# Kernel tuning notes

Measured on AMD Instinct MI355X. Metric: run time of the kernel, lower is better.

The kernel has to match this reference:

```python
import jax, jax.numpy as jnp
import numpy as np

NH = 8
QCH = 256
KCH = 256
VCH = 256


def setup_inputs() -> dict:
    key = jax.random.key(0)
    ks = jax.random.split(key, 6)
    B, C, H, W = 8, 512, 28, 28
    return {
        "inputs": jax.random.normal(ks[0], (B, C, H, W), jnp.float32),
        "inputs_st": jax.random.normal(ks[1], (B, C, H, W), jnp.float32),
        "Wq": jax.random.normal(ks[2], (QCH, C), jnp.float32) * 0.02,
        "bq": jnp.zeros((QCH,), jnp.float32),
        "Wkv": jax.random.normal(ks[3], (KCH + VCH, C), jnp.float32) * 0.02,
        "bkv": jnp.zeros((KCH + VCH,), jnp.float32),
        "Wo": jax.random.normal(ks[4], (512, VCH), jnp.float32) * 0.02,
        "bo": jnp.zeros((512,), jnp.float32),
    }


def reference(inputs, inputs_st, Wq, bq, Wkv, bkv, Wo, bo):
    B, C, H, W = inputs.shape
    dkh = KCH // NH  # scale uses k-channels per head, as in source

    # 1x1 conv projections == channel matmuls
    q = jnp.einsum('bchw,oc->bohw', inputs, Wq) + bq[None, :, None, None]
    kv = jnp.einsum('bchw,oc->bohw', inputs_st, Wkv) + bkv[None, :, None, None]
    k, v = kv[:, :KCH], kv[:, KCH:]

    # split heads: (B, Nh, ch//Nh, H, W)
    q = q.reshape(B, NH, QCH // NH, H, W) * (dkh ** -0.5)
    k = k.reshape(B, NH, KCH // NH, H, W)
    v = v.reshape(B, NH, VCH // NH, H, W)

    flat_q = q.reshape(B, NH, QCH // NH, H * W)
    flat_k = k.reshape(B, NH, KCH // NH, H * W)
    flat_v = v.reshape(B, NH, VCH // NH, H * W)

    # logits: (B, Nh, HqWq, HW) = q^T k
    logits = jnp.einsum('bnds,bndt->bnst', flat_q, flat_k)
    # NOTE: source applies softmax over dim=1 (the head axis), not the key axis
    weights = jax.nn.softmax(logits, axis=1)
    # attn_out: (B, Nh, HqWq, dvh)
    attn_out = jnp.einsum('bnst,bndt->bnsd', weights, flat_v)
    # faithful raw reshapes (no transpose), matching torch.reshape semantics
    attn_out = attn_out.reshape(B, NH, VCH // NH, H, W)
    attn_out = attn_out.reshape(B, VCH, H, W)

    out = jnp.einsum('bchw,oc->bohw', attn_out, Wo) + bo[None, :, None, None]
    return out
```

## Files before the change

kernel.cpp:

```cpp
#include <hip/hip_runtime.h>

#define SS 784
#define NQE 1605632

typedef float f32x4 __attribute__((ext_vector_type(4)));
typedef short s16x8 __attribute__((ext_vector_type(8)));

__device__ inline ushort f2bf(float f) {
    union { float f; unsigned u; } v; v.f = f;
    return (ushort)((v.u + 0x7fff + ((v.u >> 16) & 1)) >> 16);
}
__device__ inline float bf2f(ushort h) {
    union { unsigned u; float f; } v; v.u = ((unsigned)h) << 16;
    return v.f;
}
__device__ inline unsigned cvt_pk_bf16(float lo, float hi) {
    unsigned r;
    asm("v_cvt_pk_bf16_f32 %0, %1, %2" : "=v"(r) : "v"(lo), "v"(hi));
    return r;
}

__global__ __launch_bounds__(256) void gemm_qkv(const float* __restrict__ X0,
                                                const float* __restrict__ X1,
                                                const float* __restrict__ Wq,
                                                const float* __restrict__ bq,
                                                const float* __restrict__ Wkv,
                                                const float* __restrict__ bkv,
                                                ushort* __restrict__ qt,
                                                ushort* __restrict__ kt,
                                                ushort* __restrict__ vv,
                                                float qscale) {
    __shared__ ushort As[128 * 40];
    __shared__ float  Xf[32 * 68];
    const int id  = blockIdx.x;
    const int b   = id & 7;
    const int sub = id >> 3;
    const int oy  = sub % 6;
    const int p0  = (sub / 6) * 64;
    const int mode = (oy < 2) ? 0 : (oy < 4 ? 1 : 2);
    const float* X    = (mode == 0) ? X0 : X1;
    const float* Wg   = (mode == 0) ? Wq : Wkv;
    const float* bias = (mode == 0) ? bq : bkv;
    const int o0w = (mode == 0) ? oy * 128 : (oy - 2) * 128;

    const int tid = threadIdx.x;
    const int lane = tid & 63, wave = tid >> 6;
    const int wm = wave >> 1, wn = wave & 1;
    const int lg = lane >> 4, lm = lane & 15;
    const int srow = tid >> 1, shalf = (tid & 1) * 16;
    const int bc = tid >> 3;
    const int bp = (tid & 7) * 8;

    const f32x4 Z4 = {0.f, 0.f, 0.f, 0.f};
    f32x4 acc[4][2];
    #pragma unroll
    for (int m = 0; m < 4; ++m)
        #pragma unroll
        for (int n = 0; n < 2; ++n) acc[m][n] = Z4;

    const float* Xb = X + (size_t)b * 512 * SS;

    for (int c0 = 0; c0 < 512; c0 += 32) {
        __syncthreads();
        {
            const float* src = Wg + (size_t)(o0w + srow) * 512 + c0 + shalf;
            ushort tmp[16];
            #pragma unroll
            for (int jj = 0; jj < 4; ++jj) {
                float4 v = *(const float4*)(src + jj * 4);
                tmp[jj * 4 + 0] = f2bf(v.x); tmp[jj * 4 + 1] = f2bf(v.y);
                tmp[jj * 4 + 2] = f2bf(v.z); tmp[jj * 4 + 3] = f2bf(v.w);
            }
            *(s16x8*)&As[srow * 40 + shalf]     = *(s16x8*)&tmp[0];
            *(s16x8*)&As[srow * 40 + shalf + 8] = *(s16x8*)&tmp[8];
        }
        {
            const float* src = Xb + (size_t)(c0 + bc) * SS + p0 + bp;
            float* dst = &Xf[bc * 68 + bp];
            #pragma unroll
            for (int k = 0; k < 2; ++k) {
                f32x4 v = (p0 + bp + 4 * k < SS) ? *(const f32x4*)(src + 4 * k) : Z4;
                *(f32x4*)(dst + 4 * k) = v;
            }
        }
        __syncthreads();
        s16x8 af[4];
        #pragma unroll
        for (int m = 0; m < 4; ++m) af[m] = *(const s16x8*)&As[(wm * 64 + m * 16 + lm) * 40 + 8 * lg];
        #pragma unroll
        for (int n = 0; n < 2; ++n) {
            const float* col = &Xf[(8 * lg) * 68 + wn * 32 + n * 16 + lm];
            uint4 pk;
            pk.x = cvt_pk_bf16(col[0 * 68], col[1 * 68]);
            pk.y = cvt_pk_bf16(col[2 * 68], col[3 * 68]);
            pk.z = cvt_pk_bf16(col[4 * 68], col[5 * 68]);
            pk.w = cvt_pk_bf16(col[6 * 68], col[7 * 68]);
            s16x8 bf8 = *(s16x8*)&pk;
            #pragma unroll
            for (int m = 0; m < 4; ++m)
                acc[m][n] = __builtin_amdgcn_mfma_f32_16x16x32_bf16(af[m], bf8, acc[m][n], 0, 0, 0);
        }
    }

    if (mode < 2) {
        ushort* outT = (mode == 0) ? qt : kt;
        const float scale = (mode == 0) ? qscale : 1.0f;
        #pragma unroll
        for (int m = 0; m < 4; ++m) {
            const int o = o0w + wm * 64 + m * 16 + 4 * lg;
            float bv[4];
            #pragma unroll
            for (int r = 0; r < 4; ++r) bv[r] = bias[o + r];
            #pragma unroll
            for (int n = 0; n < 2; ++n) {
                const int p = p0 + wn * 32 + n * 16 + lm;
                if (p < SS) {
                    ushort4 w;
                    w.x = f2bf((acc[m][n][0] + bv[0]) * scale);
                    w.y = f2bf((acc[m][n][1] + bv[1]) * scale);
                    w.z = f2bf((acc[m][n][2] + bv[2]) * scale);
                    w.w = f2bf((acc[m][n][3] + bv[3]) * scale);
                    *(ushort4*)&outT[((size_t)b * SS + p) * 256 + o] = w;
                }
            }
        }
    } else {
        #pragma unroll
        for (int m = 0; m < 4; ++m) {
            const int ob = o0w + wm * 64 + m * 16 + 4 * lg;
            float bv[4];
            #pragma unroll
            for (int r = 0; r < 4; ++r) bv[r] = bias[ob + r];
            #pragma unroll
            for (int n = 0; n < 2; ++n) {
                const int p = p0 + wn * 32 + n * 16 + lm;
                if (p < SS) {
                    #pragma unroll
                    for (int r = 0; r < 4; ++r) {
                        const int c = ob - 256 + r;
                        vv[((size_t)b * 256 + c) * SS + p] = f2bf(acc[m][n][r] + bv[r]);
                    }
                }
            }
        }
    }
}

#define KROW 280
#define VROW 40
#define PROW 40

__global__ __launch_bounds__(256, 3) void attn_mfma(const ushort* __restrict__ qt,
                                                    const ushort* __restrict__ kt,
                                                    const ushort* __restrict__ vv,
                                                    ushort* __restrict__ pb,
                                                    ushort* __restrict__ p4) {
    __shared__ ushort ks[32 * KROW];
    __shared__ ushort vs[256 * VROW];
    __shared__ ushort pls[4 * 2 * 16 * PROW];
    const int tid  = threadIdx.x;
    const int lane = tid & 63;
    const int wave = tid >> 6;
    const int b     = blockIdx.x;
    const int stile = blockIdx.y / 5;
    const int ts    = blockIdx.y % 5;
    int strip = stile * 4 + wave;
    const bool valid = (strip < 49);
    if (!valid) strip = 48;
    const int s0 = strip * 16;

    const int lg = lane >> 4, lm = lane & 15;
    const s16x8 Z8 = {0, 0, 0, 0, 0, 0, 0, 0};
    const f32x4 Z4 = {0.f, 0.f, 0.f, 0.f};

    s16x8 qf[8];
    const ushort* qbase = qt + ((size_t)b * SS + s0 + lm) * 256 + 8 * lg;
    #pragma unroll
    for (int n = 0; n < 8; ++n) qf[n] = *(const s16x8*)(qbase + n * 32);

    f32x4 oacc[8][2];
    #pragma unroll
    for (int n = 0; n < 8; ++n) { oacc[n][0] = Z4; oacc[n][1] = Z4; }

    const ushort* ktb = kt + (size_t)b * SS * 256;
    const ushort* vb  = vv + (size_t)b * 256 * SS;
    ushort* pbase = pls + wave * (2 * 16 * PROW);

    for (int ti = ts * 5; ti < ts * 5 + 5; ++ti) {
        const int t0 = ti * 32;
        __syncthreads();
        {
            const int row = tid >> 3, ce = (tid & 7) * 32;
            const int t = t0 + row;
            const ushort* src = ktb + (size_t)t * 256 + ce;
            #pragma unroll
            for (int j = 0; j < 4; ++j) {
                s16x8 v = (t < SS) ? *(const s16x8*)(src + 8 * j) : Z8;
                *(s16x8*)&ks[row * KROW + ce + 8 * j] = v;
            }
        }
        {
            const ushort* src = vb + (size_t)tid * SS + t0;
            #pragma unroll
            for (int j = 0; j < 4; ++j) {
                s16x8 v = (t0 + 8 * j < SS) ? *(const s16x8*)(src + 8 * j) : Z8;
                *(s16x8*)&vs[tid * VROW + 8 * j] = v;
            }
        }
        __syncthreads();

        unsigned pku[2][8][2];
        #pragma unroll
        for (int h = 0; h < 2; ++h) {
            f32x4 lacc[8];
            #pragma unroll
            for (int n = 0; n < 8; ++n) {
                s16x8 ak = *(const s16x8*)&ks[(h * 16 + lm) * KROW + n * 32 + 8 * lg];
                lacc[n] = __builtin_amdgcn_mfma_f32_16x16x32_bf16(ak, qf[n], Z4, 0, 0, 0);
            }
            #pragma unroll
            for (int r = 0; r < 4; ++r) {
                float e[8]; float sum = 0.f;
                #pragma unroll
                for (int n = 0; n < 8; ++n) { e[n] = exp2f(lacc[n][r]); sum += e[n]; }
                float inv;
                asm("v_rcp_f32 %0, %1" : "=v"(inv) : "v"(sum));
                #pragma unroll
                for (int n = 0; n < 8; ++n) lacc[n][r] = e[n] * inv;
            }
            #pragma unroll
            for (int n = 0; n < 8; ++n) {
                pku[h][n][0] = cvt_pk_bf16(lacc[n][0], lacc[n][1]);
                pku[h][n][1] = cvt_pk_bf16(lacc[n][2], lacc[n][3]);
            }
        }

        #pragma unroll
        for (int n = 0; n < 8; ++n) {
            ushort* pw = pbase + (n & 1) * (16 * PROW);
            uint2 w0; w0.x = pku[0][n][0]; w0.y = pku[0][n][1];
            *(uint2*)&pw[lm * PROW + 4 * lg] = w0;
            uint2 w1; w1.x = pku[1][n][0]; w1.y = pku[1][n][1];
            *(uint2*)&pw[lm * PROW + 16 + 4 * lg] = w1;
            s16x8 pbf = *(const s16x8*)&pw[lm * PROW + 8 * lg];
            #pragma unroll
            for (int dh = 0; dh < 2; ++dh) {
                s16x8 va = *(const s16x8*)&vs[(n * 32 + dh * 16 + lm) * VROW + 8 * lg];
                oacc[n][dh] = __builtin_amdgcn_mfma_f32_16x16x32_bf16(va, pbf, oacc[n][dh], 0, 0, 0);
            }
        }
    }

    if (valid) {
        ushort* part = (ts < 4) ? (pb + (size_t)ts * NQE) : p4;
        const size_t base = (size_t)b * 200704 + (size_t)s0 * 32 + lm * 32 + 4 * lg;
        #pragma unroll
        for (int n = 0; n < 8; ++n) {
            #pragma unroll
            for (int dh = 0; dh < 2; ++dh) {
                uint2 w;
                w.x = cvt_pk_bf16(oacc[n][dh][0], oacc[n][dh][1]);
                w.y = cvt_pk_bf16(oacc[n][dh][2], oacc[n][dh][3]);
                *(uint2*)&part[base + n * 25088 + dh * 16] = w;
            }
        }
    }
}

__global__ __launch_bounds__(256) void gemm_out5(const ushort* __restrict__ a0,
                                                 const ushort* __restrict__ a1,
                                                 const ushort* __restrict__ a2,
                                                 const ushort* __restrict__ a3,
                                                 const ushort* __restrict__ a4,
                                                 const float* __restrict__ Wg,
                                                 const float* __restrict__ bias,
                                                 float* __restrict__ outp) {
    __shared__ ushort As[64 * 40];
    __shared__ ushort Bs[128 * 40];
    const int tid = threadIdx.x;
    const int lane = tid & 63, wave = tid >> 6;
    const int wm = wave >> 1, wn = wave & 1;
    const int lg = lane >> 4, lm = lane & 15;
    const int b  = blockIdx.x;
    const int p0 = blockIdx.y * 64;
    const int o0 = blockIdx.z * 128;
    const int srow = tid >> 1, shalf = (tid & 1) * 16;
    const int tc = tid >> 3;
    const int tp = (tid & 7) * 8;

    const f32x4 Z4 = {0.f, 0.f, 0.f, 0.f};
    f32x4 acc[2][4];
    #pragma unroll
    for (int m = 0; m < 2; ++m)
        #pragma unroll
        for (int n = 0; n < 4; ++n) acc[m][n] = Z4;

    for (int c0 = 0; c0 < 256; c0 += 32) {
        __syncthreads();
        {
            const int p = p0 + tp;
            if (p < SS) {
                const size_t off = ((size_t)b * 256 + c0 + tc) * SS + p;
                s16x8 v0 = *(const s16x8*)(a0 + off);
                s16x8 v1 = *(const s16x8*)(a1 + off);
                s16x8 v2 = *(const s16x8*)(a2 + off);
                s16x8 v3 = *(const s16x8*)(a3 + off);
                s16x8 v4 = *(const s16x8*)(a4 + off);
                #pragma unroll
                for (int j = 0; j < 8; ++j) {
                    float s = bf2f((ushort)v0[j]) + bf2f((ushort)v1[j]) + bf2f((ushort)v2[j])
                            + bf2f((ushort)v3[j]) + bf2f((ushort)v4[j]);
                    As[(tp + j) * 40 + tc] = f2bf(s);
                }
            } else {
                #pragma unroll
                for (int j = 0; j < 8; ++j) As[(tp + j) * 40 + tc] = 0;
            }
        }
        {
            const float* src = Wg + (size_t)(o0 + srow) * 256 + c0 + shalf;
            ushort tmp[16];
            #pragma unroll
            for (int jj = 0; jj < 4; ++jj) {
                float4 v = *(const float4*)(src + jj * 4);
                tmp[jj * 4 + 0] = f2bf(v.x); tmp[jj * 4 + 1] = f2bf(v.y);
                tmp[jj * 4 + 2] = f2bf(v.z); tmp[jj * 4 + 3] = f2bf(v.w);
            }
            *(s16x8*)&Bs[srow * 40 + shalf]     = *(s16x8*)&tmp[0];
            *(s16x8*)&Bs[srow * 40 + shalf + 8] = *(s16x8*)&tmp[8];
        }
        __syncthreads();
        s16x8 af[2], bf[4];
        #pragma unroll
        for (int m = 0; m < 2; ++m) af[m] = *(const s16x8*)&As[(wm * 32 + m * 16 + lm) * 40 + 8 * lg];
        #pragma unroll
        for (int n = 0; n < 4; ++n) bf[n] = *(const s16x8*)&Bs[(wn * 64 + n * 16 + lm) * 40 + 8 * lg];
        #pragma unroll
        for (int m = 0; m < 2; ++m)
            #pragma unroll
            for (int n = 0; n < 4; ++n)
                acc[m][n] = __builtin_amdgcn_mfma_f32_16x16x32_bf16(af[m], bf[n], acc[m][n], 0, 0, 0);
    }

    #pragma unroll
    for (int n = 0; n < 4; ++n) {
        const int o = o0 + wn * 64 + n * 16 + lm;
        const float bv = bias[o];
        #pragma unroll
        for (int m = 0; m < 2; ++m) {
            const int p = p0 + wm * 32 + m * 16 + 4 * lg;
            if (p < SS) {
                f32x4 v;
                #pragma unroll
                for (int r = 0; r < 4; ++r) v[r] = acc[m][n][r] + bv;
                *(f32x4*)&outp[((size_t)b * 512 + o) * SS + p] = v;
            }
        }
    }
}

extern "C" void kernel_launch(void* const* d_in, const int* in_sizes, int n_in,
                              void* d_out, int out_size, void* d_ws, size_t ws_size,
                              hipStream_t stream) {
    const float* inputs    = (const float*)d_in[0];
    const float* inputs_st = (const float*)d_in[1];
    const float* Wq        = (const float*)d_in[2];
    const float* bq        = (const float*)d_in[3];
    const float* Wkv       = (const float*)d_in[4];
    const float* bkv       = (const float*)d_in[5];
    const float* Wo        = (const float*)d_in[6];
    const float* bo        = (const float*)d_in[7];
    float* out = (float*)d_out;

    ushort* W     = (ushort*)d_ws;
    ushort* qt    = W + 4 * (size_t)NQE;
    ushort* kt    = W + 5 * (size_t)NQE;
    ushort* vv    = W + 6 * (size_t)NQE;
    ushort* p4    = W + 7 * (size_t)NQE;

    const float qscale = (float)(1.4426950408889634 / 5.656854249492380195);

    gemm_qkv<<<dim3(624), dim3(256), 0, stream>>>(inputs, inputs_st, Wq, bq, Wkv, bkv, qt, kt, vv, qscale);
    attn_mfma<<<dim3(8, 65), dim3(256), 0, stream>>>(qt, kt, vv, W, p4);
    gemm_out5<<<dim3(8, 13, 4), dim3(256), 0, stream>>>(W, W + (size_t)NQE, W + 2 * (size_t)NQE,
                                                        W + 3 * (size_t)NQE, p4, Wo, bo, out);
}
```

Baseline: 85.01 us.

## Drop LDS staging of K/V in attention and split key range into ten partials

The attention kernel no longer stages K and V tiles through shared memory with block barriers. Each wave now loads its MFMA fragments for K and V straight from global memory. The key dimension is split into 10 chunks instead of 5, doubling the grid to raise parallelism, and the output GEMM sums 10 bf16 partial buffers. The cost is redundant global and L2 traffic, since the four waves no longer share K/V loads, plus more partial-buffer writes and reads in the output GEMM.

```diff
diff --git a/kernel.cpp b/kernel.cpp
--- a/kernel.cpp
+++ b/kernel.cpp
@@ -146,24 +146,19 @@
     }
 }
 
-#define KROW 280
-#define VROW 40
 #define PROW 40
 
-__global__ __launch_bounds__(256, 3) void attn_mfma(const ushort* __restrict__ qt,
-                                                    const ushort* __restrict__ kt,
-                                                    const ushort* __restrict__ vv,
-                                                    ushort* __restrict__ pb,
-                                                    ushort* __restrict__ p4) {
-    __shared__ ushort ks[32 * KROW];
-    __shared__ ushort vs[256 * VROW];
-    __shared__ ushort pls[4 * 2 * 16 * PROW];
+__global__ __launch_bounds__(256) void attn_mfma(const ushort* __restrict__ qt,
+                                                 const ushort* __restrict__ kt,
+                                                 const ushort* __restrict__ vv,
+                                                 ushort* __restrict__ pb) {
+    __shared__ ushort pls[4][16 * PROW];
     const int tid  = threadIdx.x;
     const int lane = tid & 63;
     const int wave = tid >> 6;
     const int b     = blockIdx.x;
-    const int stile = blockIdx.y / 5;
-    const int ts    = blockIdx.y % 5;
+    const int stile = blockIdx.y / 10;
+    const int ts    = blockIdx.y % 10;
     int strip = stile * 4 + wave;
     const bool valid = (strip < 49);
     if (!valid) strip = 48;
@@ -184,38 +179,23 @@
 
     const ushort* ktb = kt + (size_t)b * SS * 256;
     const ushort* vb  = vv + (size_t)b * 256 * SS;
-    ushort* pbase = pls + wave * (2 * 16 * PROW);
-
-    for (int ti = ts * 5; ti < ts * 5 + 5; ++ti) {
+    ushort* pw = pls[wave];
+
+    const int nt = (ts < 5) ? 3 : 2;
+    const int tb = (ts < 5) ? ts * 3 : 15 + (ts - 5) * 2;
+
+    for (int ti = tb; ti < tb + nt; ++ti) {
         const int t0 = ti * 32;
-        __syncthreads();
-        {
-            const int row = tid >> 3, ce = (tid & 7) * 32;
-            const int t = t0 + row;
-            const ushort* src = ktb + (size_t)t * 256 + ce;
-            #pragma unroll
-            for (int j = 0; j < 4; ++j) {
-                s16x8 v = (t < SS) ? *(const s16x8*)(src + 8 * j) : Z8;
-                *(s16x8*)&ks[row * KROW + ce + 8 * j] = v;
-            }
-        }
-        {
-            const ushort* src = vb + (size_t)tid * SS + t0;
-            #pragma unroll
-            for (int j = 0; j < 4; ++j) {
-                s16x8 v = (t0 + 8 * j < SS) ? *(const s16x8*)(src + 8 * j) : Z8;
-                *(s16x8*)&vs[tid * VROW + 8 * j] = v;
-            }
-        }
-        __syncthreads();
 
         unsigned pku[2][8][2];
         #pragma unroll
         for (int h = 0; h < 2; ++h) {
+            const int t = t0 + h * 16 + lm;
+            const ushort* ksrc = ktb + (size_t)t * 256 + 8 * lg;
             f32x4 lacc[8];
             #pragma unroll
             for (int n = 0; n < 8; ++n) {
-                s16x8 ak = *(const s16x8*)&ks[(h * 16 + lm) * KROW + n * 32 + 8 * lg];
+                s16x8 ak = (t < SS) ? *(const s16x8*)(ksrc + n * 32) : Z8;
                 lacc[n] = __builtin_amdgcn_mfma_f32_16x16x32_bf16(ak, qf[n], Z4, 0, 0, 0);
             }
             #pragma unroll
@@ -235,9 +215,9 @@
             }
         }
 
+        const bool vok = (t0 + 8 * lg < SS);
         #pragma unroll
         for (int n = 0; n < 8; ++n) {
-            ushort* pw = pbase + (n & 1) * (16 * PROW);
             uint2 w0; w0.x = pku[0][n][0]; w0.y = pku[0][n][1];
             *(uint2*)&pw[lm * PROW + 4 * lg] = w0;
             uint2 w1; w1.x = pku[1][n][0]; w1.y = pku[1][n][1];
@@ -245,14 +225,15 @@
             s16x8 pbf = *(const s16x8*)&pw[lm * PROW + 8 * lg];
             #pragma unroll
             for (int dh = 0; dh < 2; ++dh) {
-                s16x8 va = *(const s16x8*)&vs[(n * 32 + dh * 16 + lm) * VROW + 8 * lg];
+                const ushort* vsrc = vb + (size_t)(n * 32 + dh * 16 + lm) * SS + t0 + 8 * lg;
+                s16x8 va = vok ? *(const s16x8*)vsrc : Z8;
                 oacc[n][dh] = __builtin_amdgcn_mfma_f32_16x16x32_bf16(va, pbf, oacc[n][dh], 0, 0, 0);
             }
         }
     }
 
     if (valid) {
-        ushort* part = (ts < 4) ? (pb + (size_t)ts * NQE) : p4;
+        ushort* part = pb + (size_t)ts * NQE;
         const size_t base = (size_t)b * 200704 + (size_t)s0 * 32 + lm * 32 + 4 * lg;
         #pragma unroll
         for (int n = 0; n < 8; ++n) {
@@ -267,11 +248,7 @@
     }
 }
 
-__global__ __launch_bounds__(256) void gemm_out5(const ushort* __restrict__ a0,
-                                                 const ushort* __restrict__ a1,
-                                                 const ushort* __restrict__ a2,
-                                                 const ushort* __restrict__ a3,
-                                                 const ushort* __restrict__ a4,
+__global__ __launch_bounds__(256) void gemm_out5(const ushort* __restrict__ pb,
                                                  const float* __restrict__ Wg,
                                                  const float* __restrict__ bias,
                                                  float* __restrict__ outp) {
@@ -301,17 +278,15 @@
             const int p = p0 + tp;
             if (p < SS) {
                 const size_t off = ((size_t)b * 256 + c0 + tc) * SS + p;
-                s16x8 v0 = *(const s16x8*)(a0 + off);
-                s16x8 v1 = *(const s16x8*)(a1 + off);
-                s16x8 v2 = *(const s16x8*)(a2 + off);
-                s16x8 v3 = *(const s16x8*)(a3 + off);
-                s16x8 v4 = *(const s16x8*)(a4 + off);
-                #pragma unroll
-                for (int j = 0; j < 8; ++j) {
-                    float s = bf2f((ushort)v0[j]) + bf2f((ushort)v1[j]) + bf2f((ushort)v2[j])
-                            + bf2f((ushort)v3[j]) + bf2f((ushort)v4[j]);
-                    As[(tp + j) * 40 + tc] = f2bf(s);
+                float s[8] = {0.f, 0.f, 0.f, 0.f, 0.f, 0.f, 0.f, 0.f};
+                #pragma unroll
+                for (int k = 0; k < 10; ++k) {
+                    s16x8 v = *(const s16x8*)(pb + (size_t)k * NQE + off);
+                    #pragma unroll
+                    for (int j = 0; j < 8; ++j) s[j] += bf2f((ushort)v[j]);
                 }
+                #pragma unroll
+                for (int j = 0; j < 8; ++j) As[(tp + j) * 40 + tc] = f2bf(s[j]);
             } else {
                 #pragma unroll
                 for (int j = 0; j < 8; ++j) As[(tp + j) * 40 + tc] = 0;
@@ -372,16 +347,14 @@
     const float* bo        = (const float*)d_in[7];
     float* out = (float*)d_out;
 
-    ushort* W     = (ushort*)d_ws;
-    ushort* qt    = W + 4 * (size_t)NQE;
-    ushort* kt    = W + 5 * (size_t)NQE;
-    ushort* vv    = W + 6 * (size_t)NQE;
-    ushort* p4    = W + 7 * (size_t)NQE;
+    ushort* W  = (ushort*)d_ws;
+    ushort* qt = W + 10 * (size_t)NQE;
+    ushort* kt = W + 11 * (size_t)NQE;
+    ushort* vv = W + 12 * (size_t)NQE;
 
     const float qscale = (float)(1.4426950408889634 / 5.656854249492380195);
 
     gemm_qkv<<<dim3(624), dim3(256), 0, stream>>>(inputs, inputs_st, Wq, bq, Wkv, bkv, qt, kt, vv, qscale);
-    attn_mfma<<<dim3(8, 65), dim3(256), 0, stream>>>(qt, kt, vv, W, p4);
-    gemm_out5<<<dim3(8, 13, 4), dim3(256), 0, stream>>>(W, W + (size_t)NQE, W + 2 * (size_t)NQE,
-                                                        W + 3 * (size_t)NQE, p4, Wo, bo, out);
-}
+    attn_mfma<<<dim3(8, 130), dim3(256), 0, stream>>>(qt, kt, vv, W);
+    gemm_out5<<<dim3(8, 13, 4), dim3(256), 0, stream>>>(W, Wo, bo, out);
+}
```

Measured after the change: 111.8 us. +31.5%, slower.
